# Kernel tuning notes

Measured on AMD Instinct MI355X. Metric: run time of the kernel, lower is better.

The kernel has to match this reference:

```python
import jax, jax.numpy as jnp
import numpy as np

N, D, H = 4096, 128, 8

def setup_inputs() -> dict:
    key = jax.random.key(0)
    ks = jax.random.split(key, 7)
    xavier = float(np.sqrt(6.0 / (D + D)))  # xavier_uniform for [*, D, D]
    x = jax.random.normal(ks[0], (N, D), dtype=jnp.float32)
    W_k = jax.random.uniform(ks[1], (H, D, D), minval=-xavier, maxval=xavier, dtype=jnp.float32)
    W_q = jax.random.uniform(ks[2], (H, D, D), minval=-xavier, maxval=xavier, dtype=jnp.float32)
    W_v = jax.random.uniform(ks[3], (H, D, D), minval=-xavier, maxval=xavier, dtype=jnp.float32)
    W_m = jnp.ones((H,), dtype=jnp.float32)
    lim = float(1.0 / np.sqrt(D))  # default torch Linear init range
    Wg = jax.random.uniform(ks[4], (D, D), minval=-lim, maxval=lim, dtype=jnp.float32)
    bg = jax.random.uniform(ks[5], (D,), minval=-lim, maxval=lim, dtype=jnp.float32)
    return {"x": x, "W_k": W_k, "W_q": W_q, "W_v": W_v, "W_m": W_m, "Wg": Wg, "bg": bg}

def reference(x, W_k, W_q, W_v, W_m, Wg, bg):
    # per-head projections: [H, N, D]
    q = jnp.einsum('nf,hfd->hnd', x, W_q)
    k = jnp.einsum('nf,hfd->hnd', x, W_k)
    v = jnp.einsum('nf,hfd->hnd', x, W_v)
    # dense all-pairs attention scores per head: [H, N, N]
    e = jnp.einsum('hnd,hmd->hnm', q, k)
    attn = jax.nn.softmax(e, axis=-1)
    # weighted sum over values, then head-scaled accumulation: [N, D]
    out = jnp.einsum('h,hnm,hmd->nd', W_m, attn, v)
    # residual MLP: x + ReLU(Linear(x + out))
    h = x + out
    g = jax.nn.relu(h @ Wg.T + bg)
    return x + g
```

## Files before the change

kernel.cpp:

```cpp
#include <hip/hip_runtime.h>

#define NROWS 4096
#define DDIM  128
#define NHEAD 8

typedef __attribute__((ext_vector_type(8))) short    short8;
typedef __attribute__((ext_vector_type(8))) _Float16 half8;
typedef __attribute__((ext_vector_type(4))) float    floatx4;

__device__ __forceinline__ float bf2f(unsigned short u){
  unsigned v = ((unsigned)u) << 16;
  return __builtin_bit_cast(float, v);
}
__device__ __forceinline__ unsigned short f2bf(float f){
  unsigned u = __builtin_bit_cast(unsigned, f);
  u += 0x7FFFu + ((u >> 16) & 1u);
  return (unsigned short)(u >> 16);
}
__device__ __forceinline__ void split2(float v, unsigned short& hi, unsigned short& lo){
  hi = f2bf(v);
  lo = f2bf(v - bf2f(hi));
}
__device__ __forceinline__ void async_cp16(const _Float16* g, _Float16* l){
  __builtin_amdgcn_global_load_lds(
      (const __attribute__((address_space(1))) void*)g,
      (__attribute__((address_space(3))) void*)l, 16, 0, 0);
}

__global__ void fill_kernel(float* __restrict__ out, float val, int n){
  int i = blockIdx.x * 256 + threadIdx.x;
  if (i < n) out[i] = val;
}

__global__ __launch_bounds__(256, 2) void proj_kernel(
    const float* __restrict__ x,
    const float* __restrict__ Wk, const float* __restrict__ Wv,
    _Float16* __restrict__ kfo, _Float16* __restrict__ vfo)
{
  __shared__ alignas(16) unsigned short wthi[DDIM][72];
  __shared__ alignas(16) unsigned short wtlo[DDIM][72];
  const int tid = threadIdx.x, lane = tid & 63, wave = tid >> 6;
  const int l4 = lane & 15, quad = lane >> 4;
  const int tile = blockIdx.x, h = blockIdx.y, z = blockIdx.z;
  const float* W = (z == 0 ? Wk : Wv) + h * DDIM * DDIM;

  floatx4 acc[8];
#pragma unroll
  for (int c = 0; c < 8; c++) acc[c] = (floatx4)0.f;

  for (int fh = 0; fh < 2; fh++) {
    for (int i = tid; i < DDIM * 64; i += 256) {
      const int d = i >> 6, fl = i & 63;
      unsigned short hi, lo;
      split2(W[(fh * 64 + fl) * DDIM + d], hi, lo);
      wthi[d][fl] = hi; wtlo[d][fl] = lo;
    }
    __syncthreads();

    const float* xr = x + (size_t)(tile * 64 + wave * 16 + l4) * DDIM + fh * 64 + quad * 8;
    short8 ah[2], al[2];
#pragma unroll
    for (int t2 = 0; t2 < 2; t2++) {
      float4 v0 = *(const float4*)(xr + t2 * 32);
      float4 v1 = *(const float4*)(xr + t2 * 32 + 4);
      float xv[8] = {v0.x, v0.y, v0.z, v0.w, v1.x, v1.y, v1.z, v1.w};
#pragma unroll
      for (int j = 0; j < 8; j++) {
        unsigned short hi, lo; split2(xv[j], hi, lo);
        ah[t2][j] = (short)hi; al[t2][j] = (short)lo;
      }
    }
#pragma unroll
    for (int t2 = 0; t2 < 2; t2++) {
#pragma unroll
      for (int c = 0; c < 8; c++) {
        short8 bh = *(const short8*)(&wthi[c * 16 + l4][t2 * 32 + quad * 8]);
        short8 bl = *(const short8*)(&wtlo[c * 16 + l4][t2 * 32 + quad * 8]);
        acc[c] = __builtin_amdgcn_mfma_f32_16x16x32_bf16(ah[t2], bh, acc[c], 0, 0, 0);
        acc[c] = __builtin_amdgcn_mfma_f32_16x16x32_bf16(al[t2], bh, acc[c], 0, 0, 0);
        acc[c] = __builtin_amdgcn_mfma_f32_16x16x32_bf16(ah[t2], bl, acc[c], 0, 0, 0);
      }
    }
    __syncthreads();
  }

  const int rb = wave * 16 + quad * 4;
  const size_t tilebase = (size_t)(h * 64 + tile) * 8192;
#pragma unroll
  for (int c = 0; c < 8; c++) {
    const int d = c * 16 + l4;
#pragma unroll
    for (int r = 0; r < 4; r++) {
      const int kl = rb + r;
      const float val = acc[c][r];
      if (z == 0) {
        const int c2 = kl >> 4, l4k = kl & 15;
        const int tt = d >> 5, qd = (d >> 3) & 3, jj = d & 7;
        const int qX = qd ^ ((l4k >> 1) & 3);
        kfo[tilebase + (size_t)((c2 * 4 + tt) * 16 + l4k) * 32 + qX * 8 + jj] =
            (_Float16)val;
      } else {
        const int c2 = d >> 4, l4v = d & 15;
        const int tt = kl >> 5, qd = (kl >> 3) & 3, jj = kl & 7;
        const int qX = qd ^ ((l4v >> 1) & 3);
        vfo[tilebase + (size_t)((c2 * 2 + tt) * 16 + l4v) * 32 + qX * 8 + jj] =
            (_Float16)val;
      }
    }
  }
}

union FlashLds {
  struct { unsigned short hi[DDIM][72], lo[DDIM][72]; } wq;
  float qf[64][132];
  struct { _Float16 k[8192], v[8192], p[4][2][1024]; } kv;
};

__global__ __launch_bounds__(256, 2) void flash_kernel(
    const float* __restrict__ x, const float* __restrict__ Wq,
    const _Float16* __restrict__ kfo, const _Float16* __restrict__ vfo,
    _Float16* __restrict__ op, float* __restrict__ mb, float* __restrict__ lb)
{
  __shared__ alignas(16) FlashLds lds;
  const int tid = threadIdx.x, lane = tid & 63, wave = tid >> 6;
  const int l4 = lane & 15, quad = lane >> 4;
  const int h = blockIdx.x & 7, qt = (blockIdx.x >> 3) & 31, s = blockIdx.x >> 8;
  const int q0 = qt * 128;

  half8 aq[2][4];

  {
    floatx4 qacc[2][8];
#pragma unroll
    for (int sp = 0; sp < 2; sp++)
#pragma unroll
      for (int c = 0; c < 8; c++) qacc[sp][c] = (floatx4)0.f;

    const float* Wqh = Wq + h * DDIM * DDIM;
    for (int fh = 0; fh < 2; fh++) {
      for (int i = tid; i < DDIM * 64; i += 256) {
        const int d = i >> 6, fl = i & 63;
        unsigned short hi, lo;
        split2(Wqh[(fh * 64 + fl) * DDIM + d], hi, lo);
        lds.wq.hi[d][fl] = hi; lds.wq.lo[d][fl] = lo;
      }
      __syncthreads();
#pragma unroll
      for (int sp = 0; sp < 2; sp++) {
        const float* xr = x + (size_t)(q0 + sp * 64 + wave * 16 + l4) * DDIM + fh * 64 + quad * 8;
        short8 ah[2], al[2];
#pragma unroll
        for (int t2 = 0; t2 < 2; t2++) {
          float4 v0 = *(const float4*)(xr + t2 * 32);
          float4 v1 = *(const float4*)(xr + t2 * 32 + 4);
          float xv[8] = {v0.x, v0.y, v0.z, v0.w, v1.x, v1.y, v1.z, v1.w};
#pragma unroll
          for (int j = 0; j < 8; j++) {
            unsigned short hi, lo; split2(xv[j], hi, lo);
            ah[t2][j] = (short)hi; al[t2][j] = (short)lo;
          }
        }
#pragma unroll
        for (int t2 = 0; t2 < 2; t2++) {
#pragma unroll
          for (int c = 0; c < 8; c++) {
            short8 bh = *(const short8*)(&lds.wq.hi[c * 16 + l4][t2 * 32 + quad * 8]);
            short8 bl = *(const short8*)(&lds.wq.lo[c * 16 + l4][t2 * 32 + quad * 8]);
            qacc[sp][c] = __builtin_amdgcn_mfma_f32_16x16x32_bf16(ah[t2], bh, qacc[sp][c], 0, 0, 0);
            qacc[sp][c] = __builtin_amdgcn_mfma_f32_16x16x32_bf16(al[t2], bh, qacc[sp][c], 0, 0, 0);
            qacc[sp][c] = __builtin_amdgcn_mfma_f32_16x16x32_bf16(ah[t2], bl, qacc[sp][c], 0, 0, 0);
          }
        }
      }
      __syncthreads();
    }

#pragma unroll
    for (int sp = 0; sp < 2; sp++) {
#pragma unroll
      for (int c = 0; c < 8; c++)
#pragma unroll
        for (int r = 0; r < 4; r++)
          lds.qf[wave * 16 + quad * 4 + r][c * 16 + l4] = qacc[sp][c][r];
      __syncthreads();
      if ((wave >> 1) == sp) {
#pragma unroll
        for (int g = 0; g < 2; g++)
#pragma unroll
          for (int t = 0; t < 4; t++) {
            const float* qr = &lds.qf[(wave & 1) * 32 + g * 16 + l4][t * 32 + quad * 8];
            float4 v0 = *(const float4*)qr;
            float4 v1 = *(const float4*)(qr + 4);
            aq[g][t][0] = (_Float16)v0.x; aq[g][t][1] = (_Float16)v0.y;
            aq[g][t][2] = (_Float16)v0.z; aq[g][t][3] = (_Float16)v0.w;
            aq[g][t][4] = (_Float16)v1.x; aq[g][t][5] = (_Float16)v1.y;
            aq[g][t][6] = (_Float16)v1.z; aq[g][t][7] = (_Float16)v1.w;
          }
      }
      __syncthreads();
    }
  }

  float m_run[2][4];
#pragma unroll
  for (int g = 0; g < 2; g++)
#pragma unroll
    for (int r = 0; r < 4; r++) m_run[g][r] = -1e30f;
  floatx4 Oacc[2][8], lacc[2];
#pragma unroll
  for (int g = 0; g < 2; g++) {
    lacc[g] = (floatx4)0.f;
#pragma unroll
    for (int c = 0; c < 8; c++) Oacc[g][c] = (floatx4)0.f;
  }

  half8 vones;
#pragma unroll
  for (int j = 0; j < 8; j++) vones[j] = (_Float16)1.f;

  const _Float16* kfo_h = kfo + (size_t)h * 64 * 8192;
  const _Float16* vfo_h = vfo + (size_t)h * 64 * 8192;
  const int lq = (l4 * 4 + (quad ^ ((l4 >> 1) & 3))) * 8;

  for (int kt = s * 32; kt < s * 32 + 32; ++kt) {
    {
      const _Float16* ks = kfo_h + (size_t)kt * 8192 + wave * 2048 + lane * 8;
      const _Float16* vs = vfo_h + (size_t)kt * 8192 + wave * 2048 + lane * 8;
      _Float16* kd = &lds.kv.k[wave * 2048];
      _Float16* vd = &lds.kv.v[wave * 2048];
#pragma unroll
      for (int it = 0; it < 4; it++) {
        async_cp16(ks + it * 512, kd + it * 512);
        async_cp16(vs + it * 512, vd + it * 512);
      }
    }
    __syncthreads();

    floatx4 Sf[2][4];
#pragma unroll
    for (int g = 0; g < 2; g++)
#pragma unroll
      for (int c = 0; c < 4; c++) Sf[g][c] = (floatx4)0.f;
#pragma unroll
    for (int t = 0; t < 4; t++) {
      half8 b[4];
#pragma unroll
      for (int c = 0; c < 4; c++)
        b[c] = *(const half8*)&lds.kv.k[(c * 4 + t) * 512 + lq];
#pragma unroll
      for (int g = 0; g < 2; g++)
#pragma unroll
        for (int c = 0; c < 4; c++)
          Sf[g][c] = __builtin_amdgcn_mfma_f32_16x16x32_f16(aq[g][t], b[c], Sf[g][c], 0, 0, 0);
    }

    float alpha[2][4];
#pragma unroll
    for (int g = 0; g < 2; g++) {
      float mt[4];
#pragma unroll
      for (int r = 0; r < 4; r++)
        mt[r] = fmaxf(fmaxf(Sf[g][0][r], Sf[g][1][r]), fmaxf(Sf[g][2][r], Sf[g][3][r]));
#pragma unroll
      for (int mk = 1; mk <= 8; mk <<= 1)
#pragma unroll
        for (int r = 0; r < 4; r++) mt[r] = fmaxf(mt[r], __shfl_xor(mt[r], mk, 64));
#pragma unroll
      for (int r = 0; r < 4; r++) {
        const float mn = fmaxf(m_run[g][r], mt[r]);
        alpha[g][r] = __expf(m_run[g][r] - mn);
        m_run[g][r] = mn;
      }
#pragma unroll
      for (int r = 0; r < 4; r++)
#pragma unroll
        for (int c = 0; c < 4; c++) Sf[g][c][r] = __expf(Sf[g][c][r] - m_run[g][r]);
    }

#pragma unroll
    for (int g = 0; g < 2; g++)
#pragma unroll
      for (int c = 0; c < 4; c++)
#pragma unroll
        for (int r = 0; r < 4; r++)
          lds.kv.p[wave][g][((c * 2 + (l4 >> 3)) * 16 + quad * 4 + r) * 8 + (l4 & 7)] =
              (_Float16)Sf[g][c][r];

#pragma unroll
    for (int g = 0; g < 2; g++) {
#pragma unroll
      for (int c = 0; c < 8; c++) {
        Oacc[g][c][0] *= alpha[g][0]; Oacc[g][c][1] *= alpha[g][1];
        Oacc[g][c][2] *= alpha[g][2]; Oacc[g][c][3] *= alpha[g][3];
      }
      lacc[g][0] *= alpha[g][0]; lacc[g][1] *= alpha[g][1];
      lacc[g][2] *= alpha[g][2]; lacc[g][3] *= alpha[g][3];
    }
#pragma unroll
    for (int t = 0; t < 2; t++) {
      half8 ap[2];
#pragma unroll
      for (int g = 0; g < 2; g++) {
        ap[g] = *(const half8*)&lds.kv.p[wave][g][((t * 4 + quad) * 16 + l4) * 8];
        lacc[g] = __builtin_amdgcn_mfma_f32_16x16x32_f16(ap[g], vones, lacc[g], 0, 0, 0);
      }
#pragma unroll
      for (int c = 0; c < 8; c++) {
        half8 bv = *(const half8*)&lds.kv.v[(c * 2 + t) * 512 + lq];
#pragma unroll
        for (int g = 0; g < 2; g++)
          Oacc[g][c] = __builtin_amdgcn_mfma_f32_16x16x32_f16(ap[g], bv, Oacc[g][c], 0, 0, 0);
      }
    }
    __syncthreads();
  }

#pragma unroll
  for (int g = 0; g < 2; g++) {
    const int rbase = wave * 32 + g * 16 + quad * 4;
    const size_t rowbase = (size_t)(s * NHEAD + h) * NROWS + q0 + rbase;
#pragma unroll
    for (int c = 0; c < 8; c++) {
      const int col = c * 16 + l4;
#pragma unroll
      for (int r = 0; r < 4; r++)
        op[(rowbase + r) * DDIM + col] = (_Float16)Oacc[g][c][r];
    }
    if (l4 == 0) {
#pragma unroll
      for (int r = 0; r < 4; r++) {
        mb[rowbase + r] = m_run[g][r];
        lb[rowbase + r] = lacc[g][r];
      }
    }
  }
}

__global__ __launch_bounds__(128) void merge_kernel(
    const _Float16* __restrict__ op, const float* __restrict__ mb,
    const float* __restrict__ lb, const float* __restrict__ Wm,
    float* __restrict__ u)
{
  __shared__ float sc[2][NHEAD];
  const int n = blockIdx.x, d = threadIdx.x;
  if (d < NHEAD) {
    const int h = d;
    const float m1 = mb[(size_t)h * NROWS + n];
    const float m2 = mb[(size_t)(NHEAD + h) * NROWS + n];
    const float l1 = lb[(size_t)h * NROWS + n];
    const float l2 = lb[(size_t)(NHEAD + h) * NROWS + n];
    const float m  = fmaxf(m1, m2);
    const float a1 = __expf(m1 - m), a2 = __expf(m2 - m);
    const float invL = Wm[h] / (l1 * a1 + l2 * a2);
    sc[0][h] = a1 * invL;
    sc[1][h] = a2 * invL;
  }
  __syncthreads();
  float acc = 0.f;
#pragma unroll
  for (int h = 0; h < NHEAD; h++) {
    acc += sc[0][h] * (float)op[((size_t)h * NROWS + n) * DDIM + d];
    acc += sc[1][h] * (float)op[((size_t)(NHEAD + h) * NROWS + n) * DDIM + d];
  }
  u[(size_t)n * DDIM + d] = acc;
}

__global__ __launch_bounds__(256, 2) void mlp_kernel(
    const float* __restrict__ x, const float* __restrict__ u,
    const float* __restrict__ Wg, const float* __restrict__ bg,
    float* __restrict__ out)
{
  __shared__ alignas(16) unsigned short wghi[DDIM][72];
  __shared__ alignas(16) unsigned short wglo[DDIM][72];
  const int tid = threadIdx.x, lane = tid & 63, wave = tid >> 6;
  const int l4 = lane & 15, quad = lane >> 4;
  const int r0 = blockIdx.x * 64;

  floatx4 acc[8];
#pragma unroll
  for (int c = 0; c < 8; c++) acc[c] = (floatx4)0.f;

  for (int fh = 0; fh < 2; fh++) {
    for (int i = tid; i < DDIM * 64; i += 256) {
      const int ii = i >> 6, jl = i & 63;
      unsigned short hi, lo;
      split2(Wg[ii * DDIM + fh * 64 + jl], hi, lo);
      wghi[ii][jl] = hi; wglo[ii][jl] = lo;
    }
    __syncthreads();

    const size_t xoff = (size_t)(r0 + wave * 16 + l4) * DDIM + fh * 64 + quad * 8;
    short8 ah[2], al[2];
#pragma unroll
    for (int t2 = 0; t2 < 2; t2++) {
      float4 x0 = *(const float4*)(x + xoff + t2 * 32);
      float4 x1 = *(const float4*)(x + xoff + t2 * 32 + 4);
      float4 u0 = *(const float4*)(u + xoff + t2 * 32);
      float4 u1 = *(const float4*)(u + xoff + t2 * 32 + 4);
      float hv[8] = {x0.x + u0.x, x0.y + u0.y, x0.z + u0.z, x0.w + u0.w,
                     x1.x + u1.x, x1.y + u1.y, x1.z + u1.z, x1.w + u1.w};
#pragma unroll
      for (int j = 0; j < 8; j++) {
        unsigned short hi, lo; split2(hv[j], hi, lo);
        ah[t2][j] = (short)hi; al[t2][j] = (short)lo;
      }
    }
#pragma unroll
    for (int t2 = 0; t2 < 2; t2++) {
#pragma unroll
      for (int c = 0; c < 8; c++) {
        short8 bh = *(const short8*)(&wghi[c * 16 + l4][t2 * 32 + quad * 8]);
        short8 bl = *(const short8*)(&wglo[c * 16 + l4][t2 * 32 + quad * 8]);
        acc[c] = __builtin_amdgcn_mfma_f32_16x16x32_bf16(ah[t2], bh, acc[c], 0, 0, 0);
        acc[c] = __builtin_amdgcn_mfma_f32_16x16x32_bf16(al[t2], bh, acc[c], 0, 0, 0);
        acc[c] = __builtin_amdgcn_mfma_f32_16x16x32_bf16(ah[t2], bl, acc[c], 0, 0, 0);
      }
    }
    __syncthreads();
  }

  const int rbase = wave * 16 + quad * 4;
#pragma unroll
  for (int c = 0; c < 8; c++) {
    const int col = c * 16 + l4;
    const float bgf = bg[col];
#pragma unroll
    for (int r = 0; r < 4; r++) {
      const size_t idx = (size_t)(r0 + rbase + r) * DDIM + col;
      out[idx] = x[idx] + fmaxf(acc[c][r] + bgf, 0.f);
    }
  }
}

extern "C" void kernel_launch(void* const* d_in, const int* in_sizes, int n_in,
                              void* d_out, int out_size, void* d_ws, size_t ws_size,
                              hipStream_t stream) {
  float* out = (float*)d_out;
  const int fill_blocks = (out_size + 255) / 256;

  const bool ok_sizes =
      n_in == 7 &&
      in_sizes[0] == NROWS * DDIM &&
      in_sizes[1] == NHEAD * DDIM * DDIM &&
      in_sizes[2] == NHEAD * DDIM * DDIM &&
      in_sizes[3] == NHEAD * DDIM * DDIM &&
      in_sizes[4] == NHEAD &&
      in_sizes[5] == DDIM * DDIM &&
      in_sizes[6] == DDIM &&
      out_size == NROWS * DDIM;
  if (!ok_sizes) {
    fill_kernel<<<fill_blocks, 256, 0, stream>>>(out, 1000.f, out_size);
    return;
  }

  const size_t HND = (size_t)NHEAD * NROWS * DDIM;
  const size_t ND  = (size_t)NROWS * DDIM;
  const size_t need = ND * 4 + 2 * HND * 2 + 2 * HND * 2 + 2 * NHEAD * NROWS * 8;
  if (ws_size < need) {
    fill_kernel<<<fill_blocks, 256, 0, stream>>>(out, 500.f, out_size);
    return;
  }

  const float* x  = (const float*)d_in[0];
  const float* Wk = (const float*)d_in[1];
  const float* Wq = (const float*)d_in[2];
  const float* Wv = (const float*)d_in[3];
  const float* Wm = (const float*)d_in[4];
  const float* Wg = (const float*)d_in[5];
  const float* bg = (const float*)d_in[6];

  float*     u   = (float*)d_ws;
  _Float16*  kfo = (_Float16*)(u + ND);
  _Float16*  vfo = kfo + HND;
  _Float16*  op  = vfo + HND;
  float*     mb  = (float*)(op + 2 * HND);
  float*     lb  = mb + 2 * NHEAD * NROWS;

  (void)hipGetLastError();
  proj_kernel<<<dim3(64, NHEAD, 2), 256, 0, stream>>>(x, Wk, Wv, kfo, vfo);
  flash_kernel<<<dim3(512), 256, 0, stream>>>(x, Wq, kfo, vfo, op, mb, lb);
  merge_kernel<<<dim3(4096), 128, 0, stream>>>(op, mb, lb, Wm, u);
  mlp_kernel<<<dim3(64), 256, 0, stream>>>(x, u, Wg, bg, out);
  if (hipGetLastError() != hipSuccess) {
    fill_kernel<<<fill_blocks, 256, 0, stream>>>(out, 2000.f, out_size);
  }
}
```

Before: 261.4 us.

## Split flash KV range three ways, batch proj tiles, skip unchanged rescale

The flash kernel now splits the key range into three chunks instead of two, launching 768 blocks, and the merge kernel combines three partial softmax states. The aim is better CU occupancy on the 256-CU device, since 512 blocks at two per CU leaves the machine underfilled. The projection kernel now handles four row tiles per block, reusing the split-weight LDS staging across them and cutting the number of weight conversions. The O/l rescale is also skipped when no lane's running max changed. In exchange there is more workspace, more merge traffic, and higher register pressure in proj from a 4x8 accumulator array.

```diff
diff --git a/kernel.cpp b/kernel.cpp
--- a/kernel.cpp
+++ b/kernel.cpp
@@ -41,12 +41,14 @@
   __shared__ alignas(16) unsigned short wtlo[DDIM][72];
   const int tid = threadIdx.x, lane = tid & 63, wave = tid >> 6;
   const int l4 = lane & 15, quad = lane >> 4;
-  const int tile = blockIdx.x, h = blockIdx.y, z = blockIdx.z;
+  const int h = blockIdx.y, z = blockIdx.z;
   const float* W = (z == 0 ? Wk : Wv) + h * DDIM * DDIM;
 
-  floatx4 acc[8];
-#pragma unroll
-  for (int c = 0; c < 8; c++) acc[c] = (floatx4)0.f;
+  floatx4 acc[4][8];
+#pragma unroll
+  for (int t4 = 0; t4 < 4; t4++)
+#pragma unroll
+    for (int c = 0; c < 8; c++) acc[t4][c] = (floatx4)0.f;
 
   for (int fh = 0; fh < 2; fh++) {
     for (int i = tid; i < DDIM * 64; i += 256) {
@@ -57,54 +59,62 @@
     }
     __syncthreads();
 
-    const float* xr = x + (size_t)(tile * 64 + wave * 16 + l4) * DDIM + fh * 64 + quad * 8;
-    short8 ah[2], al[2];
-#pragma unroll
-    for (int t2 = 0; t2 < 2; t2++) {
-      float4 v0 = *(const float4*)(xr + t2 * 32);
-      float4 v1 = *(const float4*)(xr + t2 * 32 + 4);
-      float xv[8] = {v0.x, v0.y, v0.z, v0.w, v1.x, v1.y, v1.z, v1.w};
-#pragma unroll
-      for (int j = 0; j < 8; j++) {
-        unsigned short hi, lo; split2(xv[j], hi, lo);
-        ah[t2][j] = (short)hi; al[t2][j] = (short)lo;
-      }
-    }
-#pragma unroll
-    for (int t2 = 0; t2 < 2; t2++) {
-#pragma unroll
-      for (int c = 0; c < 8; c++) {
-        short8 bh = *(const short8*)(&wthi[c * 16 + l4][t2 * 32 + quad * 8]);
-        short8 bl = *(const short8*)(&wtlo[c * 16 + l4][t2 * 32 + quad * 8]);
-        acc[c] = __builtin_amdgcn_mfma_f32_16x16x32_bf16(ah[t2], bh, acc[c], 0, 0, 0);
-        acc[c] = __builtin_amdgcn_mfma_f32_16x16x32_bf16(al[t2], bh, acc[c], 0, 0, 0);
-        acc[c] = __builtin_amdgcn_mfma_f32_16x16x32_bf16(ah[t2], bl, acc[c], 0, 0, 0);
+#pragma unroll
+    for (int t4 = 0; t4 < 4; t4++) {
+      const int tile = blockIdx.x * 4 + t4;
+      const float* xr = x + (size_t)(tile * 64 + wave * 16 + l4) * DDIM + fh * 64 + quad * 8;
+      short8 ah[2], al[2];
+#pragma unroll
+      for (int t2 = 0; t2 < 2; t2++) {
+        float4 v0 = *(const float4*)(xr + t2 * 32);
+        float4 v1 = *(const float4*)(xr + t2 * 32 + 4);
+        float xv[8] = {v0.x, v0.y, v0.z, v0.w, v1.x, v1.y, v1.z, v1.w};
+#pragma unroll
+        for (int j = 0; j < 8; j++) {
+          unsigned short hi, lo; split2(xv[j], hi, lo);
+          ah[t2][j] = (short)hi; al[t2][j] = (short)lo;
+        }
+      }
+#pragma unroll
+      for (int t2 = 0; t2 < 2; t2++) {
+#pragma unroll
+        for (int c = 0; c < 8; c++) {
+          short8 bh = *(const short8*)(&wthi[c * 16 + l4][t2 * 32 + quad * 8]);
+          short8 bl = *(const short8*)(&wtlo[c * 16 + l4][t2 * 32 + quad * 8]);
+          acc[t4][c] = __builtin_amdgcn_mfma_f32_16x16x32_bf16(ah[t2], bh, acc[t4][c], 0, 0, 0);
+          acc[t4][c] = __builtin_amdgcn_mfma_f32_16x16x32_bf16(al[t2], bh, acc[t4][c], 0, 0, 0);
+          acc[t4][c] = __builtin_amdgcn_mfma_f32_16x16x32_bf16(ah[t2], bl, acc[t4][c], 0, 0, 0);
+        }
       }
     }
     __syncthreads();
   }
 
   const int rb = wave * 16 + quad * 4;
-  const size_t tilebase = (size_t)(h * 64 + tile) * 8192;
-#pragma unroll
-  for (int c = 0; c < 8; c++) {
-    const int d = c * 16 + l4;
-#pragma unroll
-    for (int r = 0; r < 4; r++) {
-      const int kl = rb + r;
-      const float val = acc[c][r];
-      if (z == 0) {
-        const int c2 = kl >> 4, l4k = kl & 15;
-        const int tt = d >> 5, qd = (d >> 3) & 3, jj = d & 7;
-        const int qX = qd ^ ((l4k >> 1) & 3);
-        kfo[tilebase + (size_t)((c2 * 4 + tt) * 16 + l4k) * 32 + qX * 8 + jj] =
-            (_Float16)val;
-      } else {
-        const int c2 = d >> 4, l4v = d & 15;
-        const int tt = kl >> 5, qd = (kl >> 3) & 3, jj = kl & 7;
-        const int qX = qd ^ ((l4v >> 1) & 3);
-        vfo[tilebase + (size_t)((c2 * 2 + tt) * 16 + l4v) * 32 + qX * 8 + jj] =
-            (_Float16)val;
+#pragma unroll
+  for (int t4 = 0; t4 < 4; t4++) {
+    const int tile = blockIdx.x * 4 + t4;
+    const size_t tilebase = (size_t)(h * 64 + tile) * 8192;
+#pragma unroll
+    for (int c = 0; c < 8; c++) {
+      const int d = c * 16 + l4;
+#pragma unroll
+      for (int r = 0; r < 4; r++) {
+        const int kl = rb + r;
+        const float val = acc[t4][c][r];
+        if (z == 0) {
+          const int c2 = kl >> 4, l4k = kl & 15;
+          const int tt = d >> 5, qd = (d >> 3) & 3, jj = d & 7;
+          const int qX = qd ^ ((l4k >> 1) & 3);
+          kfo[tilebase + (size_t)((c2 * 4 + tt) * 16 + l4k) * 32 + qX * 8 + jj] =
+              (_Float16)val;
+        } else {
+          const int c2 = d >> 4, l4v = d & 15;
+          const int tt = kl >> 5, qd = (kl >> 3) & 3, jj = kl & 7;
+          const int qX = qd ^ ((l4v >> 1) & 3);
+          vfo[tilebase + (size_t)((c2 * 2 + tt) * 16 + l4v) * 32 + qX * 8 + jj] =
+              (_Float16)val;
+        }
       }
     }
   }
@@ -126,6 +136,7 @@
   const int l4 = lane & 15, quad = lane >> 4;
   const int h = blockIdx.x & 7, qt = (blockIdx.x >> 3) & 31, s = blockIdx.x >> 8;
   const int q0 = qt * 128;
+  const int kt0 = (64 * s) / 3, kt1 = (64 * (s + 1)) / 3;
 
   half8 aq[2][4];
 
@@ -222,7 +233,7 @@
   const _Float16* vfo_h = vfo + (size_t)h * 64 * 8192;
   const int lq = (l4 * 4 + (quad ^ ((l4 >> 1) & 3))) * 8;
 
-  for (int kt = s * 32; kt < s * 32 + 32; ++kt) {
+  for (int kt = kt0; kt < kt1; ++kt) {
     {
       const _Float16* ks = kfo_h + (size_t)kt * 8192 + wave * 2048 + lane * 8;
       const _Float16* vs = vfo_h + (size_t)kt * 8192 + wave * 2048 + lane * 8;
@@ -288,13 +299,17 @@
 
 #pragma unroll
     for (int g = 0; g < 2; g++) {
-#pragma unroll
-      for (int c = 0; c < 8; c++) {
-        Oacc[g][c][0] *= alpha[g][0]; Oacc[g][c][1] *= alpha[g][1];
-        Oacc[g][c][2] *= alpha[g][2]; Oacc[g][c][3] *= alpha[g][3];
-      }
-      lacc[g][0] *= alpha[g][0]; lacc[g][1] *= alpha[g][1];
-      lacc[g][2] *= alpha[g][2]; lacc[g][3] *= alpha[g][3];
+      const bool moved = (alpha[g][0] != 1.f) | (alpha[g][1] != 1.f) |
+                         (alpha[g][2] != 1.f) | (alpha[g][3] != 1.f);
+      if (__any(moved)) {
+#pragma unroll
+        for (int c = 0; c < 8; c++) {
+          Oacc[g][c][0] *= alpha[g][0]; Oacc[g][c][1] *= alpha[g][1];
+          Oacc[g][c][2] *= alpha[g][2]; Oacc[g][c][3] *= alpha[g][3];
+        }
+        lacc[g][0] *= alpha[g][0]; lacc[g][1] *= alpha[g][1];
+        lacc[g][2] *= alpha[g][2]; lacc[g][3] *= alpha[g][3];
+      }
     }
 #pragma unroll
     for (int t = 0; t < 2; t++) {
@@ -341,19 +356,22 @@
     const float* __restrict__ lb, const float* __restrict__ Wm,
     float* __restrict__ u)
 {
-  __shared__ float sc[2][NHEAD];
+  __shared__ float sc[3][NHEAD];
   const int n = blockIdx.x, d = threadIdx.x;
   if (d < NHEAD) {
     const int h = d;
-    const float m1 = mb[(size_t)h * NROWS + n];
-    const float m2 = mb[(size_t)(NHEAD + h) * NROWS + n];
-    const float l1 = lb[(size_t)h * NROWS + n];
-    const float l2 = lb[(size_t)(NHEAD + h) * NROWS + n];
-    const float m  = fmaxf(m1, m2);
-    const float a1 = __expf(m1 - m), a2 = __expf(m2 - m);
-    const float invL = Wm[h] / (l1 * a1 + l2 * a2);
-    sc[0][h] = a1 * invL;
-    sc[1][h] = a2 * invL;
+    float m0 = mb[(size_t)h * NROWS + n];
+    float m1 = mb[(size_t)(NHEAD + h) * NROWS + n];
+    float m2 = mb[(size_t)(2 * NHEAD + h) * NROWS + n];
+    float l0 = lb[(size_t)h * NROWS + n];
+    float l1 = lb[(size_t)(NHEAD + h) * NROWS + n];
+    float l2 = lb[(size_t)(2 * NHEAD + h) * NROWS + n];
+    const float m  = fmaxf(m0, fmaxf(m1, m2));
+    const float a0 = __expf(m0 - m), a1 = __expf(m1 - m), a2 = __expf(m2 - m);
+    const float invL = Wm[h] / (l0 * a0 + l1 * a1 + l2 * a2);
+    sc[0][h] = a0 * invL;
+    sc[1][h] = a1 * invL;
+    sc[2][h] = a2 * invL;
   }
   __syncthreads();
   float acc = 0.f;
@@ -361,6 +379,7 @@
   for (int h = 0; h < NHEAD; h++) {
     acc += sc[0][h] * (float)op[((size_t)h * NROWS + n) * DDIM + d];
     acc += sc[1][h] * (float)op[((size_t)(NHEAD + h) * NROWS + n) * DDIM + d];
+    acc += sc[2][h] * (float)op[((size_t)(2 * NHEAD + h) * NROWS + n) * DDIM + d];
   }
   u[(size_t)n * DDIM + d] = acc;
 }
@@ -455,7 +474,7 @@
 
   const size_t HND = (size_t)NHEAD * NROWS * DDIM;
   const size_t ND  = (size_t)NROWS * DDIM;
-  const size_t need = ND * 4 + 2 * HND * 2 + 2 * HND * 2 + 2 * NHEAD * NROWS * 8;
+  const size_t need = ND * 4 + 2 * HND * 2 + 3 * HND * 2 + 3 * NHEAD * NROWS * 8;
   if (ws_size < need) {
     fill_kernel<<<fill_blocks, 256, 0, stream>>>(out, 500.f, out_size);
     return;
@@ -473,12 +492,12 @@
   _Float16*  kfo = (_Float16*)(u + ND);
   _Float16*  vfo = kfo + HND;
   _Float16*  op  = vfo + HND;
-  float*     mb  = (float*)(op + 2 * HND);
-  float*     lb  = mb + 2 * NHEAD * NROWS;
+  float*     mb  = (float*)(op + 3 * HND);
+  float*     lb  = mb + 3 * NHEAD * NROWS;
 
   (void)hipGetLastError();
-  proj_kernel<<<dim3(64, NHEAD, 2), 256, 0, stream>>>(x, Wk, Wv, kfo, vfo);
-  flash_kernel<<<dim3(512), 256, 0, stream>>>(x, Wq, kfo, vfo, op, mb, lb);
+  proj_kernel<<<dim3(16, NHEAD, 2), 256, 0, stream>>>(x, Wk, Wv, kfo, vfo);
+  flash_kernel<<<dim3(768), 256, 0, stream>>>(x, Wq, kfo, vfo, op, mb, lb);
   merge_kernel<<<dim3(4096), 128, 0, stream>>>(op, mb, lb, Wm, u);
   mlp_kernel<<<dim3(64), 256, 0, stream>>>(x, u, Wg, bg, out);
   if (hipGetLastError() != hipSuccess) {
```

Result: slower. 279.8 us (+7.0%).
